# Performance work log

Hardware: AMD Instinct MI355X
Metric: run time of the kernel (lower is better)

Reference implementation:

```python
import jax, jax.numpy as jnp
import numpy as np

N, H, W = 128, 400, 400          # instances, feature canvas
MS = 28                          # mask_size = pooler_resolution*2
CT, CS = 80, 53                  # thing / stuff classes
STRIDE = 4                       # common_stride
HG, WG = 1600, 1600              # image-resolution gt panoptic
IGNORE = 255
LOSS_W = 1.0


def setup_inputs() -> dict:
    key = jax.random.key(0)
    ks = jax.random.split(key, 8)
    mask_logits = jax.random.normal(ks[0], (N, CT, MS, MS), jnp.float32)
    stuff_logit = jax.random.normal(ks[1], (CS, H, W), jnp.float32)
    thing_logit = jax.random.normal(ks[2], (CT, H, W), jnp.float32)
    # valid boxes in image pixel coords (x0,y0,x2,y2), width/height >= 16 px
    x0 = jax.random.uniform(ks[3], (N,), minval=0.0, maxval=1200.0)
    y0 = jax.random.uniform(ks[4], (N,), minval=0.0, maxval=1200.0)
    wh = jax.random.uniform(ks[5], (N, 2), minval=16.0, maxval=400.0)
    x2 = jnp.minimum(x0 + wh[:, 0], WG - 1.0)
    y2 = jnp.minimum(y0 + wh[:, 1], HG - 1.0)
    bbox = jnp.stack([x0, y0, x2, y2], axis=1).astype(jnp.float32)
    cls_idx = jax.random.randint(ks[6], (N,), 0, CT, dtype=jnp.int32)
    gt_panoptic = jax.random.randint(ks[7], (HG, WG), 0, CS + N, dtype=jnp.int32)
    return {"mask_logits": mask_logits, "stuff_logit": stuff_logit,
            "thing_logit": thing_logit, "bbox": bbox, "cls_idx": cls_idx,
            "gt_panoptic": gt_panoptic}


def _axis_sample(lo, size, grid, src_size):
    """Bilinear sampling coords along one axis (align_corners=False).
    lo: [N] box start (feat px, int); size: [N] box extent; grid: [G].
    Returns (idx0, idx1, frac) each [N, G]."""
    dst = grid[None, :].astype(jnp.float32) - lo[:, None].astype(jnp.float32)
    src = (dst + 0.5) * (src_size / size[:, None].astype(jnp.float32)) - 0.5
    f = jnp.floor(src)
    t = src - f
    i0 = jnp.clip(f, 0, src_size - 1).astype(jnp.int32)
    i1 = jnp.clip(f + 1, 0, src_size - 1).astype(jnp.int32)
    return i0, i1, t


def reference(mask_logits, stuff_logit, thing_logit, bbox, cls_idx, gt_panoptic):
    # _separate_fetch_logits: gather per-instance class channel -> [N, MS, MS]
    ml = mask_logits[jnp.arange(N), cls_idx]

    # _unmap_mask_logit_single: boxes -> feat coords (.long() == floor, boxes >= 0)
    bl = jnp.floor(bbox / STRIDE).astype(jnp.int32)
    x0b, y0b, x2b, y2b = bl[:, 0], bl[:, 1], bl[:, 2], bl[:, 3]
    hh = y2b - y0b + 1
    ww = x2b - x0b + 1
    ys = jnp.arange(H, dtype=jnp.int32)
    xs = jnp.arange(W, dtype=jnp.int32)

    i0, i1, ty = _axis_sample(y0b, hh, ys, MS)   # [N, H]
    j0, j1, tx = _axis_sample(x0b, ww, xs, MS)   # [N, W]

    # separable bilinear: rows [N, H, MS] then cols [N, H, W]
    r0 = jnp.take_along_axis(ml, jnp.broadcast_to(i0[:, :, None], (N, H, MS)), axis=1)
    r1 = jnp.take_along_axis(ml, jnp.broadcast_to(i1[:, :, None], (N, H, MS)), axis=1)
    rows = r0 * (1.0 - ty)[:, :, None] + r1 * ty[:, :, None]
    c0 = jnp.take_along_axis(rows, jnp.broadcast_to(j0[:, None, :], (N, H, W)), axis=2)
    c1 = jnp.take_along_axis(rows, jnp.broadcast_to(j1[:, None, :], (N, H, W)), axis=2)
    val = c0 * (1.0 - tx)[:, None, :] + c1 * tx[:, None, :]

    vy = (ys[None, :] >= jnp.maximum(y0b, 0)[:, None]) & (ys[None, :] <= jnp.minimum(y2b, H - 1)[:, None])
    vx = (xs[None, :] >= jnp.maximum(x0b, 0)[:, None]) & (xs[None, :] <= jnp.minimum(x2b, W - 1)[:, None])
    thing_mask_logit = jnp.where(vy[:, :, None] & vx[:, None, :], val, 0.0)

    # _crop_thing_logit_single: int()/round() based crop window
    bf = bbox / STRIDE
    cx1 = bf[:, 0].astype(jnp.int32)
    cy1 = bf[:, 1].astype(jnp.int32)
    cx2 = (jnp.round(bf[:, 2]) + 1.0).astype(jnp.int32)
    cy2 = (jnp.round(bf[:, 3]) + 1.0).astype(jnp.int32)
    my = (ys[None, :] >= cy1[:, None]) & (ys[None, :] < cy2[:, None])
    mx = (xs[None, :] >= cx1[:, None]) & (xs[None, :] < cx2[:, None])
    thing_sem_logit = jnp.where(my[:, :, None] & mx[:, None, :], thing_logit[cls_idx], 0.0)

    pan_logit = jnp.concatenate(
        [stuff_logit[None], (thing_mask_logit + thing_sem_logit)[None]], axis=1)

    # gt nearest-downsample to feat_size, then CE with ignore_index
    iy = jnp.floor(jnp.arange(H) * (HG / H)).astype(jnp.int32)
    ix = jnp.floor(jnp.arange(W) * (WG / W)).astype(jnp.int32)
    gt_ds = gt_panoptic[iy[:, None], ix[None, :]][None]          # [1, H, W]
    logp = jax.nn.log_softmax(pan_logit, axis=1)
    tgt = jnp.clip(gt_ds, 0, CS + N - 1)
    nll = -jnp.take_along_axis(logp, tgt[:, None], axis=1)[:, 0]  # [1, H, W]
    valid = gt_ds != IGNORE
    pan_loss = LOSS_W * jnp.sum(jnp.where(valid, nll, 0.0)) / jnp.maximum(
        jnp.sum(valid).astype(jnp.float32), 1.0)
    return pan_logit, pan_loss
```

## Files before the change

kernel.cpp:

```cpp
#include <hip/hip_runtime.h>
#include <math.h>

#define N_   128
#define H_   400
#define W_   400
#define MS_  28
#define CT_  80
#define CS_  53
#define HW_  (H_*W_)
#define NCH_ (CS_ + N_)
#define WG_  1600
#define IGN_ 255
#define G_   8
#define CPG_ 23
#define PPT_ 4
#define BT_  256
#define PPB_ (BT_*PPT_)
#define GX_  ((HW_ + PPB_ - 1)/PPB_)

struct NParam {
  int vy_lo, vy_hi, vx_lo, vx_hi;
  int cy1, cy2, cx1, cx2;
  float sy, sx;
  int y0b, x0b;
  int mlbase, thbase;
  int pad0, pad1;
};

__device__ float        g_acc[2];
__device__ unsigned int g_done;
__device__ float        g_lp[G_*HW_];
__device__ float        g_vt[HW_];

__device__ __forceinline__ void lse_update(float v, float& m, float& s) {
  float d = v - m;
  float e = __expf(-fabsf(d));
  s = (d > 0.0f) ? fmaf(s, e, 1.0f) : (s + e);
  m = fmaxf(m, v);
}

__global__ __launch_bounds__(256) void main_kernel(
    const float* __restrict__ mask_logits,
    const float* __restrict__ stuff_logit,
    const float* __restrict__ thing_logit,
    const float* __restrict__ bbox,
    const int*   __restrict__ cls_idx,
    const int*   __restrict__ gt,
    float* __restrict__ out)
{
  __shared__ NParam spar[N_];
  int tid = threadIdx.x;
  if (blockIdx.x == 0 && blockIdx.y == 0 && tid == 0) {
    g_acc[0] = 0.0f; g_acc[1] = 0.0f; g_done = 0u;
  }
  if (tid < N_) {
    int n = tid;
    float b0 = bbox[4*n+0]*0.25f, b1 = bbox[4*n+1]*0.25f,
          b2 = bbox[4*n+2]*0.25f, b3 = bbox[4*n+3]*0.25f;
    int x0b = (int)floorf(b0), y0b = (int)floorf(b1);
    int x2b = (int)floorf(b2), y2b = (int)floorf(b3);
    int hh = y2b - y0b + 1, ww = x2b - x0b + 1;
    NParam p;
    p.vy_lo = max(y0b, 0); p.vy_hi = min(y2b, H_-1);
    p.vx_lo = max(x0b, 0); p.vx_hi = min(x2b, W_-1);
    p.cy1 = (int)b1; p.cx1 = (int)b0;
    p.cy2 = (int)(rintf(b3) + 1.0f);
    p.cx2 = (int)(rintf(b2) + 1.0f);
    p.sy = 28.0f / (float)hh; p.sx = 28.0f / (float)ww;
    p.y0b = y0b; p.x0b = x0b;
    int cls = cls_idx[n];
    p.mlbase = (n*CT_ + cls)*(MS_*MS_);
    p.thbase = cls*HW_;
    p.pad0 = 0; p.pad1 = 0;
    spar[n] = p;
  }
  __syncthreads();

  int pix0 = (blockIdx.x*BT_ + tid)*PPT_;
  if (pix0 >= HW_) return;
  int y  = pix0 / W_;
  int xb = pix0 - y*W_;

  int grp = blockIdx.y;
  int c0 = grp*CPG_;
  int c1 = min(NCH_, c0 + CPG_);

  int tcs[PPT_];
  #pragma unroll
  for (int k = 0; k < PPT_; ++k) {
    int g = gt[y*(4*WG_) + (xb + k)*4];
    tcs[k] = min(max(g, 0), NCH_-1);
  }

  float mv[PPT_], sv[PPT_], vts[PPT_];
  #pragma unroll
  for (int k = 0; k < PPT_; ++k) { mv[k] = -INFINITY; sv[k] = 0.0f; vts[k] = 0.0f; }

  int c = c0;
  for (; c < min(c1, CS_); ++c) {
    float4 v = *(const float4*)(stuff_logit + c*HW_ + pix0);
    *(float4*)(out + c*HW_ + pix0) = v;
    float vk[4] = {v.x, v.y, v.z, v.w};
    #pragma unroll
    for (int k = 0; k < PPT_; ++k) {
      lse_update(vk[k], mv[k], sv[k]);
      if (c == tcs[k]) vts[k] = vk[k];
    }
  }
  for (; c < c1; ++c) {
    int n = c - CS_;
    NParam p = spar[n];
    float vv[PPT_] = {0.0f, 0.0f, 0.0f, 0.0f};
    if (y >= p.cy1 && y < p.cy2 && xb < p.cx2 && xb+PPT_-1 >= p.cx1) {
      float4 t = *(const float4*)(thing_logit + p.thbase + pix0);
      float tk[4] = {t.x, t.y, t.z, t.w};
      #pragma unroll
      for (int k = 0; k < PPT_; ++k) {
        int x = xb + k;
        if (x >= p.cx1 && x < p.cx2) vv[k] = tk[k];
      }
    }
    if (y >= p.vy_lo && y <= p.vy_hi && xb <= p.vx_hi && xb+PPT_-1 >= p.vx_lo) {
      float srcy = ((float)(y - p.y0b) + 0.5f)*p.sy - 0.5f;
      float fy = floorf(srcy); float ty = srcy - fy;
      int i0 = (int)fminf(fmaxf(fy,        0.0f), (float)(MS_-1));
      int i1 = (int)fminf(fmaxf(fy + 1.0f, 0.0f), (float)(MS_-1));
      const float* r0p = mask_logits + p.mlbase + i0*MS_;
      const float* r1p = mask_logits + p.mlbase + i1*MS_;
      #pragma unroll
      for (int k = 0; k < PPT_; ++k) {
        int x = xb + k;
        if (x >= p.vx_lo && x <= p.vx_hi) {
          float srcx = ((float)(x - p.x0b) + 0.5f)*p.sx - 0.5f;
          float fx = floorf(srcx); float tx = srcx - fx;
          int j0 = (int)fminf(fmaxf(fx,        0.0f), (float)(MS_-1));
          int j1 = (int)fminf(fmaxf(fx + 1.0f, 0.0f), (float)(MS_-1));
          float r0 = r0p[j0]*(1.0f - tx) + r0p[j1]*tx;
          float r1 = r1p[j0]*(1.0f - tx) + r1p[j1]*tx;
          vv[k] += r0*(1.0f - ty) + r1*ty;
        }
      }
    }
    *(float4*)(out + c*HW_ + pix0) = make_float4(vv[0], vv[1], vv[2], vv[3]);
    #pragma unroll
    for (int k = 0; k < PPT_; ++k) {
      lse_update(vv[k], mv[k], sv[k]);
      if (c == tcs[k]) vts[k] = vv[k];
    }
  }

  float4 lp = make_float4(mv[0] + __logf(sv[0]), mv[1] + __logf(sv[1]),
                          mv[2] + __logf(sv[2]), mv[3] + __logf(sv[3]));
  *(float4*)(g_lp + grp*HW_ + pix0) = lp;

  #pragma unroll
  for (int k = 0; k < PPT_; ++k)
    if (tcs[k] >= c0 && tcs[k] < c1) g_vt[pix0 + k] = vts[k];
}

__global__ __launch_bounds__(256) void reduce_kernel(
    const int* __restrict__ gt,
    float* __restrict__ out)
{
  int tid = threadIdx.x;
  int pix0 = (blockIdx.x*BT_ + tid)*PPT_;
  float nll = 0.0f, cnt = 0.0f;
  if (pix0 < HW_) {
    float4 l0 = *(const float4*)(g_lp + pix0);
    float mv[PPT_] = {l0.x, l0.y, l0.z, l0.w};
    float sv[PPT_] = {1.0f, 1.0f, 1.0f, 1.0f};
    #pragma unroll
    for (int g = 1; g < G_; ++g) {
      float4 lg4 = *(const float4*)(g_lp + g*HW_ + pix0);
      float lg[PPT_] = {lg4.x, lg4.y, lg4.z, lg4.w};
      #pragma unroll
      for (int k = 0; k < PPT_; ++k) {
        float d = lg[k] - mv[k];
        float e = __expf(-fabsf(d));
        sv[k] = (d > 0.0f) ? fmaf(sv[k], e, 1.0f) : (sv[k] + e);
        mv[k] = fmaxf(mv[k], lg[k]);
      }
    }
    float4 vt4 = *(const float4*)(g_vt + pix0);
    float vt[PPT_] = {vt4.x, vt4.y, vt4.z, vt4.w};
    int y  = pix0 / W_;
    int xb = pix0 - y*W_;
    #pragma unroll
    for (int k = 0; k < PPT_; ++k) {
      int g = gt[y*(4*WG_) + (xb + k)*4];
      bool valid = (g != IGN_);
      nll += valid ? (mv[k] + __logf(sv[k]) - vt[k]) : 0.0f;
      cnt += valid ? 1.0f : 0.0f;
    }
  }

  for (int off = 32; off >= 1; off >>= 1) {
    nll += __shfl_down(nll, off, 64);
    cnt += __shfl_down(cnt, off, 64);
  }
  __shared__ float red[8];
  int lane = tid & 63, wid = tid >> 6;
  if (lane == 0) { red[wid*2] = nll; red[wid*2+1] = cnt; }
  __syncthreads();
  if (tid == 0) {
    float ts  = red[0] + red[2] + red[4] + red[6];
    float tcn = red[1] + red[3] + red[5] + red[7];
    atomicAdd(&g_acc[0], ts);
    atomicAdd(&g_acc[1], tcn);
    __threadfence();
    unsigned int d = atomicAdd(&g_done, 1u);
    if (d == gridDim.x - 1) {
      __threadfence();
      float loss = g_acc[0] / fmaxf(g_acc[1], 1.0f);
      out[NCH_*HW_] = loss;
    }
  }
}

extern "C" void kernel_launch(void* const* d_in, const int* in_sizes, int n_in,
                              void* d_out, int out_size, void* d_ws, size_t ws_size,
                              hipStream_t stream) {
  const float* mask_logits = (const float*)d_in[0];
  const float* stuff_logit = (const float*)d_in[1];
  const float* thing_logit = (const float*)d_in[2];
  const float* bbox        = (const float*)d_in[3];
  const int*   cls_idx     = (const int*)d_in[4];
  const int*   gt          = (const int*)d_in[5];
  float* out = (float*)d_out;

  dim3 grid1(GX_, G_);
  main_kernel<<<grid1, BT_, 0, stream>>>(mask_logits, stuff_logit, thing_logit,
                                         bbox, cls_idx, gt, out);
  reduce_kernel<<<GX_, BT_, 0, stream>>>(gt, out);
}
```

Baseline: 224.4 us.

## Skip out-of-box instance channels, use nontemporal IO, gather target logit in reduce

```diff
diff --git a/kernel.cpp b/kernel.cpp
--- a/kernel.cpp
+++ b/kernel.cpp
@@ -17,6 +17,9 @@
 #define BT_  256
 #define PPB_ (BT_*PPT_)
 #define GX_  ((HW_ + PPB_ - 1)/PPB_)
+#define RB_  (HW_/BT_)
+
+typedef float f4 __attribute__((ext_vector_type(4)));
 
 struct NParam {
   int vy_lo, vy_hi, vx_lo, vx_hi;
@@ -30,7 +33,6 @@
 __device__ float        g_acc[2];
 __device__ unsigned int g_done;
 __device__ float        g_lp[G_*HW_];
-__device__ float        g_vt[HW_];
 
 __device__ __forceinline__ void lse_update(float v, float& m, float& s) {
   float d = v - m;
@@ -45,10 +47,10 @@
     const float* __restrict__ thing_logit,
     const float* __restrict__ bbox,
     const int*   __restrict__ cls_idx,
-    const int*   __restrict__ gt,
     float* __restrict__ out)
 {
   __shared__ NParam spar[N_];
+  __shared__ int4   sbox[N_];
   int tid = threadIdx.x;
   if (blockIdx.x == 0 && blockIdx.y == 0 && tid == 0) {
     g_acc[0] = 0.0f; g_acc[1] = 0.0f; g_done = 0u;
@@ -73,6 +75,8 @@
     p.thbase = cls*HW_;
     p.pad0 = 0; p.pad1 = 0;
     spar[n] = p;
+    sbox[n] = make_int4(min(p.vy_lo, p.cy1), max(p.vy_hi, p.cy2 - 1),
+                        min(p.vx_lo, p.cx1), max(p.vx_hi, p.cx2 - 1));
   }
   __syncthreads();
 
@@ -85,39 +89,36 @@
   int c0 = grp*CPG_;
   int c1 = min(NCH_, c0 + CPG_);
 
-  int tcs[PPT_];
+  float mv[PPT_], sv[PPT_];
   #pragma unroll
-  for (int k = 0; k < PPT_; ++k) {
-    int g = gt[y*(4*WG_) + (xb + k)*4];
-    tcs[k] = min(max(g, 0), NCH_-1);
-  }
-
-  float mv[PPT_], sv[PPT_], vts[PPT_];
-  #pragma unroll
-  for (int k = 0; k < PPT_; ++k) { mv[k] = -INFINITY; sv[k] = 0.0f; vts[k] = 0.0f; }
+  for (int k = 0; k < PPT_; ++k) { mv[k] = -INFINITY; sv[k] = 0.0f; }
+  int zc = 0;
 
   int c = c0;
   for (; c < min(c1, CS_); ++c) {
-    float4 v = *(const float4*)(stuff_logit + c*HW_ + pix0);
-    *(float4*)(out + c*HW_ + pix0) = v;
-    float vk[4] = {v.x, v.y, v.z, v.w};
+    f4 v = __builtin_nontemporal_load((const f4*)(stuff_logit + c*HW_ + pix0));
+    __builtin_nontemporal_store(v, (f4*)(out + c*HW_ + pix0));
     #pragma unroll
-    for (int k = 0; k < PPT_; ++k) {
-      lse_update(vk[k], mv[k], sv[k]);
-      if (c == tcs[k]) vts[k] = vk[k];
-    }
+    for (int k = 0; k < PPT_; ++k) lse_update(v[k], mv[k], sv[k]);
   }
   for (; c < c1; ++c) {
     int n = c - CS_;
+    int4 u = sbox[n];
+    float* op = out + c*HW_ + pix0;
+    if (y < u.x || y > u.y || xb > u.w || xb + PPT_ - 1 < u.z) {
+      f4 z = {0.0f, 0.0f, 0.0f, 0.0f};
+      __builtin_nontemporal_store(z, (f4*)op);
+      ++zc;
+      continue;
+    }
     NParam p = spar[n];
     float vv[PPT_] = {0.0f, 0.0f, 0.0f, 0.0f};
     if (y >= p.cy1 && y < p.cy2 && xb < p.cx2 && xb+PPT_-1 >= p.cx1) {
-      float4 t = *(const float4*)(thing_logit + p.thbase + pix0);
-      float tk[4] = {t.x, t.y, t.z, t.w};
+      f4 t = __builtin_nontemporal_load((const f4*)(thing_logit + p.thbase + pix0));
       #pragma unroll
       for (int k = 0; k < PPT_; ++k) {
         int x = xb + k;
-        if (x >= p.cx1 && x < p.cx2) vv[k] = tk[k];
+        if (x >= p.cx1 && x < p.cx2) vv[k] = t[k];
       }
     }
     if (y >= p.vy_lo && y <= p.vy_hi && xb <= p.vx_hi && xb+PPT_-1 >= p.vx_lo) {
@@ -141,21 +142,24 @@
         }
       }
     }
-    *(float4*)(out + c*HW_ + pix0) = make_float4(vv[0], vv[1], vv[2], vv[3]);
+    f4 ov = {vv[0], vv[1], vv[2], vv[3]};
+    __builtin_nontemporal_store(ov, (f4*)op);
     #pragma unroll
-    for (int k = 0; k < PPT_; ++k) {
-      lse_update(vv[k], mv[k], sv[k]);
-      if (c == tcs[k]) vts[k] = vv[k];
-    }
-  }
-
-  float4 lp = make_float4(mv[0] + __logf(sv[0]), mv[1] + __logf(sv[1]),
-                          mv[2] + __logf(sv[2]), mv[3] + __logf(sv[3]));
-  *(float4*)(g_lp + grp*HW_ + pix0) = lp;
-
+    for (int k = 0; k < PPT_; ++k) lse_update(vv[k], mv[k], sv[k]);
+  }
+
+  float zcf = (float)zc;
+  f4 lp;
   #pragma unroll
-  for (int k = 0; k < PPT_; ++k)
-    if (tcs[k] >= c0 && tcs[k] < c1) g_vt[pix0 + k] = vts[k];
+  for (int k = 0; k < PPT_; ++k) {
+    float m = mv[k], s = sv[k];
+    if (zc > 0) {
+      if (m >= 0.0f) { s = fmaf(zcf, __expf(-m), s); }
+      else           { s = fmaf(s, __expf(m), zcf); m = 0.0f; }
+    }
+    lp[k] = m + __logf(s);
+  }
+  *(f4*)(g_lp + grp*HW_ + pix0) = lp;
 }
 
 __global__ __launch_bounds__(256) void reduce_kernel(
@@ -163,36 +167,25 @@
     float* __restrict__ out)
 {
   int tid = threadIdx.x;
-  int pix0 = (blockIdx.x*BT_ + tid)*PPT_;
-  float nll = 0.0f, cnt = 0.0f;
-  if (pix0 < HW_) {
-    float4 l0 = *(const float4*)(g_lp + pix0);
-    float mv[PPT_] = {l0.x, l0.y, l0.z, l0.w};
-    float sv[PPT_] = {1.0f, 1.0f, 1.0f, 1.0f};
-    #pragma unroll
-    for (int g = 1; g < G_; ++g) {
-      float4 lg4 = *(const float4*)(g_lp + g*HW_ + pix0);
-      float lg[PPT_] = {lg4.x, lg4.y, lg4.z, lg4.w};
-      #pragma unroll
-      for (int k = 0; k < PPT_; ++k) {
-        float d = lg[k] - mv[k];
-        float e = __expf(-fabsf(d));
-        sv[k] = (d > 0.0f) ? fmaf(sv[k], e, 1.0f) : (sv[k] + e);
-        mv[k] = fmaxf(mv[k], lg[k]);
-      }
-    }
-    float4 vt4 = *(const float4*)(g_vt + pix0);
-    float vt[PPT_] = {vt4.x, vt4.y, vt4.z, vt4.w};
-    int y  = pix0 / W_;
-    int xb = pix0 - y*W_;
-    #pragma unroll
-    for (int k = 0; k < PPT_; ++k) {
-      int g = gt[y*(4*WG_) + (xb + k)*4];
-      bool valid = (g != IGN_);
-      nll += valid ? (mv[k] + __logf(sv[k]) - vt[k]) : 0.0f;
-      cnt += valid ? 1.0f : 0.0f;
-    }
-  }
+  int pix = blockIdx.x*BT_ + tid;
+  float m = g_lp[pix];
+  float s = 1.0f;
+  #pragma unroll
+  for (int g = 1; g < G_; ++g) {
+    float lg = g_lp[g*HW_ + pix];
+    float d = lg - m;
+    float e = __expf(-fabsf(d));
+    s = (d > 0.0f) ? fmaf(s, e, 1.0f) : (s + e);
+    m = fmaxf(m, lg);
+  }
+  int y = pix / W_;
+  int x = pix - y*W_;
+  int gv = gt[y*(4*WG_) + x*4];
+  int tc = min(max(gv, 0), NCH_-1);
+  float vt = out[tc*HW_ + pix];
+  bool valid = (gv != IGN_);
+  float nll = valid ? (m + __logf(s) - vt) : 0.0f;
+  float cnt = valid ? 1.0f : 0.0f;
 
   for (int off = 32; off >= 1; off >>= 1) {
     nll += __shfl_down(nll, off, 64);
@@ -230,6 +223,6 @@
 
   dim3 grid1(GX_, G_);
   main_kernel<<<grid1, BT_, 0, stream>>>(mask_logits, stuff_logit, thing_logit,
-                                         bbox, cls_idx, gt, out);
-  reduce_kernel<<<GX_, BT_, 0, stream>>>(gt, out);
-}
+                                         bbox, cls_idx, out);
+  reduce_kernel<<<RB_, BT_, 0, stream>>>(gt, out);
+}
```

Result: slower. 244.5 us (+8.9%).
